# Kernel optimization log

Hardware: AMD Instinct MI355X
Metric: run time of the kernel (lower is better)

## Reference

```python
import jax, jax.numpy as jnp
import numpy as np

EPS = 1e-5
HEADS = 8
SR = 4


def bn(x, gamma, beta, mean, var):
    # BatchNorm in inference form; channel axis = 1
    shape = (1, -1) + (1,) * (x.ndim - 2)
    inv = gamma.reshape(shape) / jnp.sqrt(var.reshape(shape) + EPS)
    return (x - mean.reshape(shape)) * inv + beta.reshape(shape)


def setup_inputs() -> dict:
    key = jax.random.key(0)
    ks = jax.random.split(key, 8)
    B, C, H, W = 2, 256, 128, 128
    N = H * W
    conv1d_std = np.sqrt(2.0 / C)            # fan_out = 1*C
    conv2d_std = np.sqrt(2.0 / (SR * SR * C))  # fan_out = sr*sr*C
    return {
        "x": jax.random.normal(ks[0], (B, C, N), dtype=jnp.float32),
        "w_q": jax.random.normal(ks[1], (C, C), dtype=jnp.float32) * conv1d_std,
        "w_k": jax.random.normal(ks[2], (C, C), dtype=jnp.float32) * conv1d_std,
        "w_sr": jax.random.normal(ks[3], (C, C, SR, SR), dtype=jnp.float32) * conv2d_std,
        "sr_gamma": jnp.ones((C,), jnp.float32),
        "sr_beta": jnp.zeros((C,), jnp.float32),
        "sr_mean": jnp.zeros((C,), jnp.float32),
        "sr_var": jnp.ones((C,), jnp.float32),
        "w_proj": jax.random.normal(ks[4], (C, C), dtype=jnp.float32) * conv1d_std,
        "proj_gamma": jnp.ones((C,), jnp.float32),
        "proj_beta": jnp.zeros((C,), jnp.float32),
        "proj_mean": jnp.zeros((C,), jnp.float32),
        "proj_var": jnp.ones((C,), jnp.float32),
        "H": 128,
        "W": 128,
    }


def reference(x, w_q, w_k, w_sr, sr_gamma, sr_beta, sr_mean, sr_var,
              w_proj, proj_gamma, proj_beta, proj_mean, proj_var, H, W):
    B, C, N = x.shape
    hd = C // HEADS
    scale = hd ** -0.5
    # q: Conv1d(k=1) == channel matmul -> (B, heads, N, hd)
    q = jnp.einsum('oc,bcn->bon', w_q, x).reshape(B, HEADS, hd, N).transpose(0, 1, 3, 2)
    # spatial reduction: Conv2d(k=SR, s=SR) as patch-reshape + einsum, then BN
    xp = x.reshape(B, C, H // SR, SR, W // SR, SR)
    xr = jnp.einsum('bchpwq,ocpq->bohw', xp, w_sr).reshape(B, C, (H // SR) * (W // SR))
    xr = bn(xr, sr_gamma, sr_beta, sr_mean, sr_var)
    # k: (B, heads, hd, N_kv)
    k = jnp.einsum('oc,bcm->bom', w_k, xr).reshape(B, HEADS, hd, -1)
    # scores (B, heads, N, N_kv) -> max over kv
    scores = jnp.einsum('bhnd,bhdm->bhnm', q, k) * scale
    attn = scores.max(axis=-1)                # (B, heads, N)
    # v = mean-pooled x, identical per head -> matmul collapses to sum over heads
    v = x.mean(axis=-1)                       # (B, C)
    out = jnp.einsum('bhn,bc->bcn', attn, v)  # (B, C, N)
    out = jnp.einsum('oc,bcn->bon', w_proj, out)
    return bn(out, proj_gamma, proj_beta, proj_mean, proj_var)
```

## Files before the change

### kernel.cpp

```cpp
#include <hip/hip_runtime.h>
#include <hip/hip_bf16.h>
#include <math.h>

#define EPSF 1e-5f
#define SCALE 0.17677669529663687f

typedef __bf16 bf16x8 __attribute__((ext_vector_type(8)));
typedef float f32x4 __attribute__((ext_vector_type(4)));


__global__ __launch_bounds__(256) void k_stage0(const float* __restrict__ wq,
                                                const float* __restrict__ wk,
                                                const float* __restrict__ wsr,
                                                const float* __restrict__ x,
                                                __bf16* __restrict__ wqf,
                                                __bf16* __restrict__ wkb,
                                                __bf16* __restrict__ wsrf,
                                                __bf16* __restrict__ Pbf,
                                                __bf16* __restrict__ xTf,
                                                float* __restrict__ vpart,
                                                float* __restrict__ ssg) {
    const int bi = blockIdx.x, t = threadIdx.x;
    if (bi >= 1120) {
        __shared__ float ts[32 * 68];
        __shared__ float sv[256];
        const int bid = bi - 1120;
        const int b = bid >> 8, n0 = (bid & 255) << 6;
        const int nl = t >> 2;
        const int ch = (t & 3) << 3;
        const int n = n0 + nl;
        const int ntile = n >> 4, ln = n & 15, quad = ch >> 3;
        const int cl = t >> 3;
        const int n8 = (t & 7) << 3;
        sv[t] = 0.f;
        for (int s8 = 0; s8 < 8; ++s8) {
            const int c0 = s8 << 5;
            __syncthreads();
            {
                const float* src = &x[((size_t)(b * 256 + c0 + cl) << 14) + n0 + n8];
                float4 a0 = *(const float4*)&src[0];
                float4 a1 = *(const float4*)&src[4];
                *(float4*)&ts[cl * 68 + n8] = a0;
                *(float4*)&ts[cl * 68 + n8 + 4] = a1;
                atomicAdd(&sv[c0 + cl],
                          a0.x + a0.y + a0.z + a0.w + a1.x + a1.y + a1.z + a1.w);
            }
            __syncthreads();
            bf16x8 p;
#pragma unroll
            for (int j = 0; j < 8; ++j) p[j] = (__bf16)ts[(ch + j) * 68 + nl];
            *(bf16x8*)&xTf[(((((size_t)(b * 1024 + ntile) << 3) + s8) << 6) +
                            (quad << 4) + ln) << 3] = p;
        }
        __syncthreads();
        vpart[(bid << 8) + t] = sv[t];
        return;
    }
    if (bi >= 608) {
        const int bid = bi - 608;
        const int b = bid >> 8, hm = (bid >> 3) & 31, ccg = bid & 7;
        const int wm = t >> 3, c8 = t & 7;
        const int mtile = (hm << 1) + (wm >> 4);
        const int ln = wm & 15;
#pragma unroll
        for (int cci = 0; cci < 4; ++cci) {
            const int c = (ccg << 5) + (cci << 3) + c8;
            const float* src = x + ((size_t)(b * 256 + c) << 14) + (hm << 9) + (wm << 2);
            bf16x8 o0, o1;
#pragma unroll
            for (int p = 0; p < 2; ++p) {
                float4 vv = *(const float4*)&src[p << 7];
                o0[p * 4 + 0] = (__bf16)vv.x; o0[p * 4 + 1] = (__bf16)vv.y;
                o0[p * 4 + 2] = (__bf16)vv.z; o0[p * 4 + 3] = (__bf16)vv.w;
            }
#pragma unroll
            for (int p = 0; p < 2; ++p) {
                float4 vv = *(const float4*)&src[(p + 2) << 7];
                o1[p * 4 + 0] = (__bf16)vv.x; o1[p * 4 + 1] = (__bf16)vv.y;
                o1[p * 4 + 2] = (__bf16)vv.z; o1[p * 4 + 3] = (__bf16)vv.w;
            }
            size_t d0 = (((((size_t)(b * 64 + mtile) << 7) + (c >> 1)) << 6) +
                         (((c & 1) << 1) << 4) + ln) << 3;
            *(bf16x8*)&Pbf[d0] = o0;
            *(bf16x8*)&Pbf[d0 + 128] = o1;
        }
        return;
    }
    if (bi >= 576) {
        int e = (bi - 576) * 256 + t;
        *(float4*)&ssg[e << 2] = make_float4(0.f, 0.f, 0.f, 0.f);
        return;
    }
    if (bi < 32) {
        int tt = bi * 256 + t;
        int o = tt >> 5, chunk = tt & 31;
        float4 v0 = *(const float4*)&wq[o * 256 + (chunk << 3)];
        float4 v1 = *(const float4*)&wq[o * 256 + (chunk << 3) + 4];
        bf16x8 p;
        p[0] = (__bf16)v0.x; p[1] = (__bf16)v0.y; p[2] = (__bf16)v0.z; p[3] = (__bf16)v0.w;
        p[4] = (__bf16)v1.x; p[5] = (__bf16)v1.y; p[6] = (__bf16)v1.z; p[7] = (__bf16)v1.w;
        int cc = chunk >> 2, quad = chunk & 3;
        *(bf16x8*)&wqf[(((((o >> 4) << 3) + cc) << 6) + (quad << 4) + (o & 15)) << 3] = p;
    } else if (bi < 64) {
        int e = (bi - 32) * 256 + t;
        float4 v0 = *(const float4*)&wk[e << 3];
        float4 v1 = *(const float4*)&wk[(e << 3) + 4];
        bf16x8 p;
        p[0] = (__bf16)(v0.x * SCALE); p[1] = (__bf16)(v0.y * SCALE);
        p[2] = (__bf16)(v0.z * SCALE); p[3] = (__bf16)(v0.w * SCALE);
        p[4] = (__bf16)(v1.x * SCALE); p[5] = (__bf16)(v1.y * SCALE);
        p[6] = (__bf16)(v1.z * SCALE); p[7] = (__bf16)(v1.w * SCALE);
        *(bf16x8*)&wkb[e << 3] = p;
    } else {
        int tt = (bi - 64) * 256 + t;
        int o = tt >> 9, chunk = tt & 511;
        float4 v0 = *(const float4*)&wsr[o * 4096 + (chunk << 3)];
        float4 v1 = *(const float4*)&wsr[o * 4096 + (chunk << 3) + 4];
        bf16x8 p;
        p[0] = (__bf16)v0.x; p[1] = (__bf16)v0.y; p[2] = (__bf16)v0.z; p[3] = (__bf16)v0.w;
        p[4] = (__bf16)v1.x; p[5] = (__bf16)v1.y; p[6] = (__bf16)v1.z; p[7] = (__bf16)v1.w;
        int cc = chunk >> 2, quad = chunk & 3;
        *(bf16x8*)&wsrf[(((((o >> 4) << 7) + cc) << 6) + (quad << 4) + (o & 15)) << 3] = p;
    }
}

__global__ __launch_bounds__(256) void k_mm1(const __bf16* __restrict__ Pbf,
                                             const __bf16* __restrict__ wsrf,
                                             const float* __restrict__ sg,
                                             const float* __restrict__ sb,
                                             const float* __restrict__ smn,
                                             const float* __restrict__ svar,
                                             __bf16* __restrict__ xrb,
                                             const __bf16* __restrict__ xTf,
                                             const __bf16* __restrict__ wqf,
                                             __bf16* __restrict__ qbf) {
    const int t = threadIdx.x, bid = blockIdx.x;
    const int w = t >> 6, lane = t & 63, ln = lane & 15, quad = lane >> 4;
    if (bid < 512) {
        const int b = bid & 1, mt = (bid >> 1) & 63, og = bid >> 7;
        f32x4 acc = (f32x4){0.f, 0.f, 0.f, 0.f};
        const __bf16* pa = Pbf + ((size_t)(b * 64 + mt) << 16) + (lane << 3);
        const __bf16* pbm = wsrf + ((size_t)(og * 4 + w) << 16) + (lane << 3);
#pragma unroll 8
        for (int cc = 0; cc < 128; ++cc) {
            bf16x8 af = *(const bf16x8*)&pa[cc << 9];
            bf16x8 bf = *(const bf16x8*)&pbm[cc << 9];
            acc = __builtin_amdgcn_mfma_f32_16x16x32_bf16(af, bf, acc, 0, 0, 0);
        }
        const int o = (og << 6) + (w << 4) + ln;
        float inv = sg[o] / sqrtf(svar[o] + EPSF);
        float mn = smn[o], bt = sb[o];
#pragma unroll
        for (int r = 0; r < 4; ++r) {
            int m = (mt << 4) + (quad << 2) + r;
            xrb[(((size_t)b << 10) + m) * 256 + o] = (__bf16)((acc[r] - mn) * inv + bt);
        }
    } else {
        const int cid = bid - 512;
        const int b = cid >> 8, n0 = (cid & 255) << 6;
        const __bf16* pa = xTf + ((size_t)(b * 1024 + (n0 >> 4) + w) << 12) + (lane << 3);
        bf16x8 af[8];
#pragma unroll
        for (int cc = 0; cc < 8; ++cc) af[cc] = *(const bf16x8*)&pa[cc << 9];
        __bf16* qdst = qbf + (((size_t)(b << 14) + n0 + (w << 4) + (quad << 2)) << 8) + ln;
#pragma unroll
        for (int ot = 0; ot < 16; ++ot) {
            const __bf16* pbm = wqf + ((size_t)ot << 12) + (lane << 3);
            f32x4 acc = (f32x4){0.f, 0.f, 0.f, 0.f};
#pragma unroll
            for (int cc = 0; cc < 8; ++cc) {
                bf16x8 bf = *(const bf16x8*)&pbm[cc << 9];
                acc = __builtin_amdgcn_mfma_f32_16x16x32_bf16(af[cc], bf, acc, 0, 0, 0);
            }
#pragma unroll
            for (int r = 0; r < 4; ++r)
                qdst[(size_t)(r << 8) + (ot << 4)] = (__bf16)acc[r];
        }
    }
}

__global__ __launch_bounds__(256) void k_kmat2(const __bf16* __restrict__ xrb,
                                               const __bf16* __restrict__ wkb,
                                               __bf16* __restrict__ kkbh,
                                               const float* __restrict__ vpart,
                                               const float* __restrict__ wproj,
                                               const float* __restrict__ pg,
                                               const float* __restrict__ pb,
                                               const float* __restrict__ pm,
                                               const float* __restrict__ pvar,
                                               float* __restrict__ A,
                                               float* __restrict__ B0) {
    const int t = threadIdx.x, bid = blockIdx.x;
    if (bid >= 128) {
        __shared__ float vl[256];
        int b = bid - 128;
        float s0 = 0.f;
        const float* vp = vpart + ((size_t)b << 16) + t;
#pragma unroll 8
        for (int j = 0; j < 256; ++j) s0 += vp[j << 8];
        vl[t] = s0 * (1.0f / 16384.0f);
        __syncthreads();
        const float* wr = wproj + t * 256;
        float s = 0.f;
#pragma unroll 8
        for (int c = 0; c < 256; c += 4) {
            float4 w4 = *(const float4*)&wr[c];
            s += w4.x * vl[c] + w4.y * vl[c + 1] + w4.z * vl[c + 2] + w4.w * vl[c + 3];
        }
        float inv = pg[t] / sqrtf(pvar[t] + EPSF);
        A[b * 256 + t] = s * inv;
        if (b == 0) B0[t] = pb[t] - pm[t] * inv;
        return;
    }
    const int b = bid >> 6, mt = bid & 63;
    const int w = t >> 6, lane = t & 63, ln = lane & 15, quad = lane >> 4;
    f32x4 acc[4];
#pragma unroll
    for (int ot = 0; ot < 4; ++ot) acc[ot] = (f32x4){0.f, 0.f, 0.f, 0.f};
    const __bf16* pa = xrb + ((((size_t)b << 10) + (mt << 4) + ln) << 8) + (quad << 3);
    const __bf16* pbm = wkb + (((w << 6) + ln) << 8) + (quad << 3);
#pragma unroll
    for (int cc = 0; cc < 8; ++cc) {
        const int cb = cc << 5;
        bf16x8 af = *(const bf16x8*)&pa[cb];
        bf16x8 bfr[4];
#pragma unroll
        for (int ot = 0; ot < 4; ++ot) bfr[ot] = *(const bf16x8*)&pbm[(ot << 12) + cb];
#pragma unroll
        for (int ot = 0; ot < 4; ++ot)
            acc[ot] = __builtin_amdgcn_mfma_f32_16x16x32_bf16(af, bfr[ot], acc[ot], 0, 0, 0);
    }
#pragma unroll
    for (int ot = 0; ot < 4; ++ot)
#pragma unroll
        for (int r = 0; r < 4; ++r) {
            int m = (mt << 4) + (quad << 2) + r;
            int h = (w << 1) + (ot >> 1);
            int d = ((ot & 1) << 4) + ln;
            kkbh[(((size_t)(b * 8 + h)) << 15) + (m << 5) + d] = (__bf16)acc[ot][r];
        }
}

__global__ __launch_bounds__(256) void k_scores3(const __bf16* __restrict__ qbf,
                                                 const __bf16* __restrict__ kkbh,
                                                 float* __restrict__ ssg) {
    __shared__ __align__(16) __bf16 qs[64 * 72];
    __shared__ float smax[512];
    const int t = threadIdx.x;
    const int w = t >> 6;
    const int lane = t & 63;
    const int ln = lane & 15;
    const int quad = lane >> 4;
    const int bx = blockIdx.x;
    const int hp = bx & 3;
    const int n0 = ((bx >> 2) & 255) << 6;
    const int b = bx >> 10;

#pragma unroll
    for (int i = 0; i < 2; ++i) {
        const int e = t + (i << 8);
        const int row = e >> 3, o8 = (e & 7) << 3;
        bf16x8 p = *(const bf16x8*)&qbf[(((size_t)(b << 14) + n0 + row) << 8) +
                                        (hp << 6) + o8];
        *(bf16x8*)&qs[row * 72 + o8] = p;
    }
    __syncthreads();

    const f32x4 zf = {0.f, 0.f, 0.f, 0.f};
#pragma unroll
    for (int hl = 0; hl < 2; ++hl) {
        const int h = (hp << 1) + hl;
        bf16x8 qb[4];
#pragma unroll
        for (int nt = 0; nt < 4; ++nt)
            qb[nt] = *(const bf16x8*)&qs[((nt << 4) + ln) * 72 + (hl << 5) + (quad << 3)];
        const __bf16* kb_base = kkbh + ((size_t)(b * 8 + h) << 15) + (ln << 5) + (quad << 3);
        bf16x8 kb[16];
#pragma unroll
        for (int i = 0; i < 16; ++i)
            kb[i] = *(const bf16x8*)&kb_base[((w << 8) + (i << 4)) << 5];
        float rmx[4] = {-INFINITY, -INFINITY, -INFINITY, -INFINITY};
        __builtin_amdgcn_s_setprio(1);
#pragma unroll
        for (int i = 0; i < 16; ++i)
#pragma unroll
            for (int nt = 0; nt < 4; ++nt) {
                f32x4 d = __builtin_amdgcn_mfma_f32_16x16x32_bf16(kb[i], qb[nt], zf, 0, 0, 0);
                float t1 = fmaxf(fmaxf(d[0], d[1]), d[2]);
                rmx[nt] = fmaxf(fmaxf(t1, d[3]), rmx[nt]);
            }
        __builtin_amdgcn_s_setprio(0);
#pragma unroll
        for (int nt = 0; nt < 4; ++nt) {
            rmx[nt] = fmaxf(rmx[nt], __shfl_xor(rmx[nt], 16, 64));
            rmx[nt] = fmaxf(rmx[nt], __shfl_xor(rmx[nt], 32, 64));
        }
        if (lane < 16) {
#pragma unroll
            for (int nt = 0; nt < 4; ++nt)
                smax[(w << 7) + (hl << 6) + (nt << 4) + lane] = rmx[nt];
        }
    }
    __syncthreads();
    if (t < 64) {
        float s0 = fmaxf(fmaxf(smax[t], smax[128 + t]), fmaxf(smax[256 + t], smax[384 + t]));
        float s1 = fmaxf(fmaxf(smax[64 + t], smax[192 + t]),
                         fmaxf(smax[320 + t], smax[448 + t]));
        atomicAdd(&ssg[(b << 14) + n0 + t], s0 + s1);
    }
}

__global__ __launch_bounds__(256) void k_epi(const float* __restrict__ ssg,
                                             const float* __restrict__ A,
                                             const float* __restrict__ B0,
                                             float* __restrict__ out) {
    __shared__ float ss[64], sA[256], sB[256];
    const int t = threadIdx.x, bid = blockIdx.x;
    const int b = bid >> 8, n0 = (bid & 255) << 6;
    if (t < 64) ss[t] = ssg[(b << 14) + n0 + t];
    sA[t] = A[b * 256 + t];
    sB[t] = B0[t];
    __syncthreads();
#pragma unroll
    for (int i = 0; i < 16; ++i) {
        int e = t + (i << 8);
        int c = e >> 4, n4 = (e & 15) << 2;
        float4 s4 = *(const float4*)&ss[n4];
        float a = sA[c], bb = sB[c];
        float4 o4 = make_float4(fmaf(a, s4.x, bb), fmaf(a, s4.y, bb),
                                fmaf(a, s4.z, bb), fmaf(a, s4.w, bb));
        *(float4*)&out[((size_t)(b * 256 + c) << 14) + n0 + n4] = o4;
    }
}

extern "C" void kernel_launch(void* const* d_in, const int* in_sizes, int n_in,
                              void* d_out, int out_size, void* d_ws, size_t ws_size,
                              hipStream_t stream) {
    const float* x    = (const float*)d_in[0];
    const float* wq   = (const float*)d_in[1];
    const float* wk   = (const float*)d_in[2];
    const float* wsr  = (const float*)d_in[3];
    const float* sg   = (const float*)d_in[4];
    const float* sb   = (const float*)d_in[5];
    const float* smn  = (const float*)d_in[6];
    const float* svr  = (const float*)d_in[7];
    const float* wproj= (const float*)d_in[8];
    const float* pg   = (const float*)d_in[9];
    const float* pb   = (const float*)d_in[10];
    const float* pm   = (const float*)d_in[11];
    const float* pvr  = (const float*)d_in[12];
    float* out = (float*)d_out;

    char* W = (char*)d_ws;
    float*  w_vpart = (float*) (W + 0);
    float*  w_A     = (float*) (W + 524288);
    float*  w_B0    = (float*) (W + 528384);
    float*  w_ssg   = (float*) (W + 532480);
    __bf16* w_wqf   = (__bf16*)(W + 663552);
    __bf16* w_wkb   = (__bf16*)(W + 794624);
    __bf16* w_wsrf  = (__bf16*)(W + 925696);
    __bf16* w_xrb   = (__bf16*)(W + 3022848);
    __bf16* w_kkbh  = (__bf16*)(W + 3547136);
    __bf16* w_qbf   = (__bf16*)(W + 4595712);
    __bf16* w_Pbf   = (__bf16*)(W + 21372928);
    __bf16* w_xTf   = (__bf16*)(W + 38150144);

    k_stage0<<<1632, 256, 0, stream>>>(wq, wk, wsr, x, w_wqf, w_wkb, w_wsrf,
                                       w_Pbf, w_xTf, w_vpart, w_ssg);
    k_mm1<<<1024, 256, 0, stream>>>(w_Pbf, w_wsrf, sg, sb, smn, svr, w_xrb,
                                    w_xTf, w_wqf, w_qbf);
    k_kmat2<<<130, 256, 0, stream>>>(w_xrb, w_wkb, w_kkbh, w_vpart, wproj,
                                     pg, pb, pm, pvr, w_A, w_B0);
    k_scores3<<<2048, 256, 0, stream>>>(w_qbf, w_kkbh, w_ssg);
    k_epi<<<512, 256, 0, stream>>>(w_ssg, w_A, w_B0, out);
}
```

Baseline: 214.6 us.

## Fuse Q projection into scores kernel, dropping the Q intermediate buffer

The Q projection GEMM moves out of the conv kernel and into the scores kernel. Each scores block now computes its own 64x64 Q tile (two heads) from xT and the weights straight into shared memory, instead of reading a precomputed bf16 Q from global memory. This removes the write and read of a roughly 16MB Q buffer and shrinks the first GEMM launch. The cost is extra MFMA and weight-load work at the start of every scores block, which lengthens the serial prologue before the score loop.

```diff
diff --git a/kernel.cpp b/kernel.cpp
--- a/kernel.cpp
+++ b/kernel.cpp
@@ -124,58 +124,32 @@
     }
 }
 
-__global__ __launch_bounds__(256) void k_mm1(const __bf16* __restrict__ Pbf,
-                                             const __bf16* __restrict__ wsrf,
-                                             const float* __restrict__ sg,
-                                             const float* __restrict__ sb,
-                                             const float* __restrict__ smn,
-                                             const float* __restrict__ svar,
-                                             __bf16* __restrict__ xrb,
-                                             const __bf16* __restrict__ xTf,
-                                             const __bf16* __restrict__ wqf,
-                                             __bf16* __restrict__ qbf) {
+__global__ __launch_bounds__(256) void k_conv1f(const __bf16* __restrict__ Pbf,
+                                                const __bf16* __restrict__ wsrf,
+                                                const float* __restrict__ sg,
+                                                const float* __restrict__ sb,
+                                                const float* __restrict__ smn,
+                                                const float* __restrict__ svar,
+                                                __bf16* __restrict__ xrb) {
     const int t = threadIdx.x, bid = blockIdx.x;
+    const int b = bid & 1, mt = (bid >> 1) & 63, og = bid >> 7;
     const int w = t >> 6, lane = t & 63, ln = lane & 15, quad = lane >> 4;
-    if (bid < 512) {
-        const int b = bid & 1, mt = (bid >> 1) & 63, og = bid >> 7;
-        f32x4 acc = (f32x4){0.f, 0.f, 0.f, 0.f};
-        const __bf16* pa = Pbf + ((size_t)(b * 64 + mt) << 16) + (lane << 3);
-        const __bf16* pbm = wsrf + ((size_t)(og * 4 + w) << 16) + (lane << 3);
+    f32x4 acc = (f32x4){0.f, 0.f, 0.f, 0.f};
+    const __bf16* pa = Pbf + ((size_t)(b * 64 + mt) << 16) + (lane << 3);
+    const __bf16* pbm = wsrf + ((size_t)(og * 4 + w) << 16) + (lane << 3);
 #pragma unroll 8
-        for (int cc = 0; cc < 128; ++cc) {
-            bf16x8 af = *(const bf16x8*)&pa[cc << 9];
-            bf16x8 bf = *(const bf16x8*)&pbm[cc << 9];
-            acc = __builtin_amdgcn_mfma_f32_16x16x32_bf16(af, bf, acc, 0, 0, 0);
-        }
-        const int o = (og << 6) + (w << 4) + ln;
-        float inv = sg[o] / sqrtf(svar[o] + EPSF);
-        float mn = smn[o], bt = sb[o];
-#pragma unroll
-        for (int r = 0; r < 4; ++r) {
-            int m = (mt << 4) + (quad << 2) + r;
-            xrb[(((size_t)b << 10) + m) * 256 + o] = (__bf16)((acc[r] - mn) * inv + bt);
-        }
-    } else {
-        const int cid = bid - 512;
-        const int b = cid >> 8, n0 = (cid & 255) << 6;
-        const __bf16* pa = xTf + ((size_t)(b * 1024 + (n0 >> 4) + w) << 12) + (lane << 3);
-        bf16x8 af[8];
-#pragma unroll
-        for (int cc = 0; cc < 8; ++cc) af[cc] = *(const bf16x8*)&pa[cc << 9];
-        __bf16* qdst = qbf + (((size_t)(b << 14) + n0 + (w << 4) + (quad << 2)) << 8) + ln;
-#pragma unroll
-        for (int ot = 0; ot < 16; ++ot) {
-            const __bf16* pbm = wqf + ((size_t)ot << 12) + (lane << 3);
-            f32x4 acc = (f32x4){0.f, 0.f, 0.f, 0.f};
-#pragma unroll
-            for (int cc = 0; cc < 8; ++cc) {
-                bf16x8 bf = *(const bf16x8*)&pbm[cc << 9];
-                acc = __builtin_amdgcn_mfma_f32_16x16x32_bf16(af[cc], bf, acc, 0, 0, 0);
-            }
-#pragma unroll
-            for (int r = 0; r < 4; ++r)
-                qdst[(size_t)(r << 8) + (ot << 4)] = (__bf16)acc[r];
-        }
+    for (int cc = 0; cc < 128; ++cc) {
+        bf16x8 af = *(const bf16x8*)&pa[cc << 9];
+        bf16x8 bf = *(const bf16x8*)&pbm[cc << 9];
+        acc = __builtin_amdgcn_mfma_f32_16x16x32_bf16(af, bf, acc, 0, 0, 0);
+    }
+    const int o = (og << 6) + (w << 4) + ln;
+    float inv = sg[o] / sqrtf(svar[o] + EPSF);
+    float mn = smn[o], bt = sb[o];
+#pragma unroll
+    for (int r = 0; r < 4; ++r) {
+        int m = (mt << 4) + (quad << 2) + r;
+        xrb[(((size_t)b << 10) + m) * 256 + o] = (__bf16)((acc[r] - mn) * inv + bt);
     }
 }
 
@@ -241,7 +215,8 @@
         }
 }
 
-__global__ __launch_bounds__(256) void k_scores3(const __bf16* __restrict__ qbf,
+__global__ __launch_bounds__(256) void k_scores2(const __bf16* __restrict__ xTf,
+                                                 const __bf16* __restrict__ wqf,
                                                  const __bf16* __restrict__ kkbh,
                                                  float* __restrict__ ssg) {
     __shared__ __align__(16) __bf16 qs[64 * 72];
@@ -256,14 +231,27 @@
     const int n0 = ((bx >> 2) & 255) << 6;
     const int b = bx >> 10;
 
-#pragma unroll
-    for (int i = 0; i < 2; ++i) {
-        const int e = t + (i << 8);
-        const int row = e >> 3, o8 = (e & 7) << 3;
-        bf16x8 p = *(const bf16x8*)&qbf[(((size_t)(b << 14) + n0 + row) << 8) +
-                                        (hp << 6) + o8];
-        *(bf16x8*)&qs[row * 72 + o8] = p;
-    }
+    f32x4 acc[4];
+#pragma unroll
+    for (int ot = 0; ot < 4; ++ot) acc[ot] = (f32x4){0.f, 0.f, 0.f, 0.f};
+    const __bf16* pa = xTf + ((size_t)(b * 1024 + (n0 >> 4) + w) << 12) + (lane << 3);
+    const __bf16* pbm = wqf + ((size_t)(hp << 2) << 12) + (lane << 3);
+#pragma unroll 2
+    for (int cc = 0; cc < 8; ++cc) {
+        const int cb = cc << 9;
+        bf16x8 af = *(const bf16x8*)&pa[cb];
+        bf16x8 bfr[4];
+#pragma unroll
+        for (int ot = 0; ot < 4; ++ot) bfr[ot] = *(const bf16x8*)&pbm[(ot << 12) + cb];
+#pragma unroll
+        for (int ot = 0; ot < 4; ++ot)
+            acc[ot] = __builtin_amdgcn_mfma_f32_16x16x32_bf16(af, bfr[ot], acc[ot], 0, 0, 0);
+    }
+#pragma unroll
+    for (int ot = 0; ot < 4; ++ot)
+#pragma unroll
+        for (int r = 0; r < 4; ++r)
+            qs[((w << 4) + (quad << 2) + r) * 72 + (ot << 4) + ln] = (__bf16)acc[ot][r];
     __syncthreads();
 
     const f32x4 zf = {0.f, 0.f, 0.f, 0.f};
@@ -361,16 +349,14 @@
     __bf16* w_wsrf  = (__bf16*)(W + 925696);
     __bf16* w_xrb   = (__bf16*)(W + 3022848);
     __bf16* w_kkbh  = (__bf16*)(W + 3547136);
-    __bf16* w_qbf   = (__bf16*)(W + 4595712);
-    __bf16* w_Pbf   = (__bf16*)(W + 21372928);
-    __bf16* w_xTf   = (__bf16*)(W + 38150144);
+    __bf16* w_Pbf   = (__bf16*)(W + 4595712);
+    __bf16* w_xTf   = (__bf16*)(W + 21372928);
 
     k_stage0<<<1632, 256, 0, stream>>>(wq, wk, wsr, x, w_wqf, w_wkb, w_wsrf,
                                        w_Pbf, w_xTf, w_vpart, w_ssg);
-    k_mm1<<<1024, 256, 0, stream>>>(w_Pbf, w_wsrf, sg, sb, smn, svr, w_xrb,
-                                    w_xTf, w_wqf, w_qbf);
+    k_conv1f<<<512, 256, 0, stream>>>(w_Pbf, w_wsrf, sg, sb, smn, svr, w_xrb);
     k_kmat2<<<130, 256, 0, stream>>>(w_xrb, w_wkb, w_kkbh, w_vpart, wproj,
                                      pg, pb, pm, pvr, w_A, w_B0);
-    k_scores3<<<2048, 256, 0, stream>>>(w_qbf, w_kkbh, w_ssg);
+    k_scores2<<<2048, 256, 0, stream>>>(w_xTf, w_wqf, w_kkbh, w_ssg);
     k_epi<<<512, 256, 0, stream>>>(w_ssg, w_A, w_B0, out);
 }
```

Result: faster. 202.4 us (-5.7%).
